# Performance work log

Measured on AMD Instinct MI355X. Metric: run time of the kernel, lower is better.

Reference implementation:

```python
import jax, jax.numpy as jnp
import numpy as np

B, K, H, W = 4096, 8, 64, 64   # z: [B, K, H, W], K = n_bits
S = 50                          # min(50, H*W*K) random sites sampled
HID = 64
CTX = 9 * K - 1                 # 3x3 neighborhood * K bits, minus the center-self bit


def setup_inputs() -> dict:
    key = jax.random.key(0)
    kz, k1, k2, kb, ki, kj = jax.random.split(key, 6)
    # z is a field of bits (0/1) as floats, as the (pred != z) comparison implies
    z = (jax.random.uniform(kz, (B, K, H, W)) > 0.5).astype(jnp.float32)
    W1 = jax.random.normal(k1, (CTX, HID), dtype=jnp.float32) * (1.0 / np.sqrt(CTX))
    b1 = jnp.zeros((HID,), dtype=jnp.float32)
    W2 = jax.random.normal(k2, (HID,), dtype=jnp.float32) * (1.0 / np.sqrt(HID))
    b2 = jnp.zeros((), dtype=jnp.float32)
    # the 50 random (bit, row, col) triples, precomputed (replaces torch.randint().item() loop)
    b_idx = jax.random.randint(kb, (S,), 0, K)
    i_idx = jax.random.randint(ki, (S,), 0, H)
    j_idx = jax.random.randint(kj, (S,), 0, W)
    return {"z": z, "W1": W1, "b1": b1, "W2": W2, "b2": b2,
            "b_idx": b_idx, "i_idx": i_idx, "j_idx": j_idx}


def reference(z, W1, b1, W2, b2, b_idx, i_idx, j_idx):
    # 3x3 toroidal neighborhood offsets, in the same (di outer, dj inner) order as the torch loop
    di = jnp.repeat(jnp.array([-1, 0, 1]), 3)          # [9]
    dj = jnp.tile(jnp.array([-1, 0, 1]), 3)            # [9]
    ni = (i_idx[:, None] + di[None, :]) % H            # [S, 9]
    nj = (j_idx[:, None] + dj[None, :]) % W            # [S, 9]

    # gather neighborhoods for all samples at once: [B, K, S, 9]
    neigh = z[:, :, ni, nj]
    # torch ctx ordering: position-major (di,dj), bit-minor -> [B, S, 9, K] -> [B, S, 9K]
    ctx_full = jnp.transpose(neigh, (0, 2, 3, 1)).reshape(z.shape[0], S, 9 * K)

    # drop the center-self entry at flat index 4*K + b (center position is the 5th of 9)
    drop = 4 * K + b_idx                               # [S]
    t = jnp.arange(CTX)                                # [CTX]
    gidx = t[None, :] + (t[None, :] >= drop[:, None])  # [S, CTX], skips `drop` per sample
    ctx = jnp.take_along_axis(ctx_full, gidx[None, :, :], axis=2)  # [B, S, CTX]

    # tiny 2-layer MLP predictor, batched over all B*S contexts
    h = jax.nn.relu(jnp.einsum('bsc,ch->bsh', ctx, W1) + b1)       # [B, S, HID]
    logits = jnp.einsum('bsh,h->bs', h, W2) + b2                   # [B, S]
    pred = (logits > 0).astype(z.dtype)

    target = z[:, b_idx, i_idx, j_idx]                             # [B, S]
    v = (pred != target).astype(z.dtype).mean(axis=0)              # [S] per-sample violation rate
    return v.mean()
```

## Files before the change

kernel.cpp:

```cpp
#include <hip/hip_runtime.h>

#define NB   4096
#define NK   8
#define NH   64
#define NW   64
#define NS   50
#define NHID 64
#define NCTX 71


__device__ __forceinline__ int getbit(const unsigned long long* bits, int cell) {
    int word = ((cell >> 8) << 2) | (cell & 3);
    int bit  = (cell >> 2) & 63;
    return (int)((bits[word] >> bit) & 1ull);
}

__global__ __launch_bounds__(256, 4)
void local_energy_kernel(const float* __restrict__ z,
                         const float* __restrict__ W1,
                         const float* __restrict__ b1,
                         const float* __restrict__ W2,
                         const float* __restrict__ b2,
                         const int*   __restrict__ b_idx,
                         const int*   __restrict__ i_idx,
                         const int*   __restrict__ j_idx,
                         float*       __restrict__ out)
{
    __shared__ unsigned long long bits[512];
    __shared__ float blocksum[4];

    const int tid  = threadIdx.x;
    const int lane = tid & 63;
    const int wave = tid >> 6;
    const int b    = blockIdx.x;

    const float4* src = (const float4*)(z + (size_t)b * (NK * NH * NW));
    for (int outer = 0; outer < 8; ++outer) {
        float4 v[4];
        #pragma unroll
        for (int q = 0; q < 4; ++q)
            v[q] = src[(outer * 4 + q) * 256 + tid];
        #pragma unroll
        for (int q = 0; q < 4; ++q) {
            int iter = outer * 4 + q;
            unsigned long long m0 = __ballot(v[q].x > 0.5f);
            unsigned long long m1 = __ballot(v[q].y > 0.5f);
            unsigned long long m2 = __ballot(v[q].z > 0.5f);
            unsigned long long m3 = __ballot(v[q].w > 0.5f);
            if (lane == 0) {
                int g = (iter << 2) | wave;
                bits[(g << 2) | 0] = m0;
                bits[(g << 2) | 1] = m1;
                bits[(g << 2) | 2] = m2;
                bits[(g << 2) | 3] = m3;
            }
        }
    }
    __syncthreads();

    float W1c[NCTX];
    #pragma unroll
    for (int t = 0; t < NCTX; ++t) W1c[t] = W1[t * NHID + lane];
    const float b1v = b1[lane];
    const float W2v = W2[lane];
    const float b2v = b2[0];

    float miss = 0.0f;
    for (int s = wave; s < NS; s += 4) {
        const int bb = b_idx[s];
        const int ii = i_idx[s];
        const int jj = j_idx[s];

        int u  = lane;
        int p  = u >> 3, k = u & 7;
        int di = p / 3, dj = p - di * 3;
        int ni = (ii + di - 1) & (NH - 1);
        int nj = (jj + dj - 1) & (NW - 1);
        int cell = (k << 12) | (ni << 6) | nj;
        unsigned long long lo = __ballot(getbit(bits, cell) != 0);

        int k2  = lane & 7;
        int ni2 = (ii + 1) & (NH - 1);
        int nj2 = (jj + 1) & (NW - 1);
        int cell2 = (k2 << 12) | (ni2 << 6) | nj2;
        int bv2 = (lane < 8) ? getbit(bits, cell2) : 0;
        unsigned long long hi = __ballot(bv2 != 0) & 0xffull;

        const int drop = 32 + bb;
        unsigned long long mlo = (lo & ((1ull << drop) - 1ull))
                               | ((lo >> (drop + 1)) << drop)
                               | ((hi & 1ull) << 63);
        unsigned int mhi = (unsigned int)(hi >> 1);

        float h0 = b1v, h1 = 0.0f, h2 = 0.0f, h3 = 0.0f;
        #pragma unroll
        for (int t = 0; t < 64; t += 4) {
            h0 += ((mlo >> (t + 0)) & 1ull) ? W1c[t + 0] : 0.0f;
            h1 += ((mlo >> (t + 1)) & 1ull) ? W1c[t + 1] : 0.0f;
            h2 += ((mlo >> (t + 2)) & 1ull) ? W1c[t + 2] : 0.0f;
            h3 += ((mlo >> (t + 3)) & 1ull) ? W1c[t + 3] : 0.0f;
        }
        #pragma unroll
        for (int t = 0; t < 7; ++t)
            h0 += ((mhi >> t) & 1u) ? W1c[64 + t] : 0.0f;
        float h = fmaxf((h0 + h1) + (h2 + h3), 0.0f);

        float c = h * W2v;
        #pragma unroll
        for (int off = 32; off >= 1; off >>= 1)
            c += __shfl_xor(c, off, 64);
        float logit = c + b2v;

        int pred = (logit > 0.0f) ? 1 : 0;
        int cellT = (bb << 12) | (ii << 6) | jj;
        int targ  = getbit(bits, cellT);
        if (lane == 0) miss += (float)(pred != targ);
    }

    if (lane == 0) blocksum[wave] = miss;
    __syncthreads();
    if (tid == 0) {
        float tot = (blocksum[0] + blocksum[1]) + (blocksum[2] + blocksum[3]);
        atomicAdd(out, tot * (1.0f / (float)(NB * NS)));
    }
}

extern "C" void kernel_launch(void* const* d_in, const int* in_sizes, int n_in,
                              void* d_out, int out_size, void* d_ws, size_t ws_size,
                              hipStream_t stream) {
    const float* z    = (const float*)d_in[0];
    const float* W1   = (const float*)d_in[1];
    const float* b1   = (const float*)d_in[2];
    const float* W2   = (const float*)d_in[3];
    const float* b2   = (const float*)d_in[4];
    const int*   b_i  = (const int*)d_in[5];
    const int*   i_i  = (const int*)d_in[6];
    const int*   j_i  = (const int*)d_in[7];
    float* out = (float*)d_out;

    hipMemsetAsync(out, 0, sizeof(float), stream);

    local_energy_kernel<<<NB, 256, 0, stream>>>(z, W1, b1, W2, b2, b_i, i_i, j_i, out);
}
```

Before: 737.0 us.

## Use nontemporal z loads, stage sample indices in LDS, two-pass reduction

Loads of z now use nontemporal loads because each element is read only once, which spares cache pollution. The sample indices are staged once per block into shared memory and the per-lane neighborhood offsets are hoisted out of the loop. The memset plus 4096 global atomics are replaced by per-block partials written to the workspace and a second single-block reduction kernel. This adds an extra kernel launch. The kernel is bound by streaming 512 MB of z, so the gains are likely marginal.

```diff
diff --git a/kernel.cpp b/kernel.cpp
--- a/kernel.cpp
+++ b/kernel.cpp
@@ -8,6 +8,7 @@
 #define NHID 64
 #define NCTX 71
 
+typedef float f32x4 __attribute__((ext_vector_type(4)));
 
 __device__ __forceinline__ int getbit(const unsigned long long* bits, int cell) {
     int word = ((cell >> 8) << 2) | (cell & 3);
@@ -24,9 +25,10 @@
                          const int*   __restrict__ b_idx,
                          const int*   __restrict__ i_idx,
                          const int*   __restrict__ j_idx,
-                         float*       __restrict__ out)
+                         float*       __restrict__ partials)
 {
     __shared__ unsigned long long bits[512];
+    __shared__ int   sidx[3][NS];
     __shared__ float blocksum[4];
 
     const int tid  = threadIdx.x;
@@ -34,19 +36,25 @@
     const int wave = tid >> 6;
     const int b    = blockIdx.x;
 
-    const float4* src = (const float4*)(z + (size_t)b * (NK * NH * NW));
+    if (tid < 3 * NS) {
+        int a = tid / NS, r = tid - a * NS;
+        const int* p = (a == 0) ? b_idx : (a == 1) ? i_idx : j_idx;
+        sidx[a][r] = p[r];
+    }
+
+    const f32x4* src = (const f32x4*)(z + (size_t)b * (NK * NH * NW));
     for (int outer = 0; outer < 8; ++outer) {
-        float4 v[4];
+        f32x4 v[4];
         #pragma unroll
         for (int q = 0; q < 4; ++q)
-            v[q] = src[(outer * 4 + q) * 256 + tid];
+            v[q] = __builtin_nontemporal_load(&src[(outer * 4 + q) * 256 + tid]);
         #pragma unroll
         for (int q = 0; q < 4; ++q) {
             int iter = outer * 4 + q;
-            unsigned long long m0 = __ballot(v[q].x > 0.5f);
-            unsigned long long m1 = __ballot(v[q].y > 0.5f);
-            unsigned long long m2 = __ballot(v[q].z > 0.5f);
-            unsigned long long m3 = __ballot(v[q].w > 0.5f);
+            unsigned long long m0 = __ballot(v[q][0] > 0.5f);
+            unsigned long long m1 = __ballot(v[q][1] > 0.5f);
+            unsigned long long m2 = __ballot(v[q][2] > 0.5f);
+            unsigned long long m3 = __ballot(v[q][3] > 0.5f);
             if (lane == 0) {
                 int g = (iter << 2) | wave;
                 bits[(g << 2) | 0] = m0;
@@ -65,24 +73,24 @@
     const float W2v = W2[lane];
     const float b2v = b2[0];
 
+    const int p  = lane >> 3;
+    const int kk = lane & 7;
+    const int di = p / 3, dj = p - di * 3;
+
     float miss = 0.0f;
     for (int s = wave; s < NS; s += 4) {
-        const int bb = b_idx[s];
-        const int ii = i_idx[s];
-        const int jj = j_idx[s];
+        const int bb = sidx[0][s];
+        const int ii = sidx[1][s];
+        const int jj = sidx[2][s];
 
-        int u  = lane;
-        int p  = u >> 3, k = u & 7;
-        int di = p / 3, dj = p - di * 3;
         int ni = (ii + di - 1) & (NH - 1);
         int nj = (jj + dj - 1) & (NW - 1);
-        int cell = (k << 12) | (ni << 6) | nj;
+        int cell = (kk << 12) | (ni << 6) | nj;
         unsigned long long lo = __ballot(getbit(bits, cell) != 0);
 
-        int k2  = lane & 7;
         int ni2 = (ii + 1) & (NH - 1);
         int nj2 = (jj + 1) & (NW - 1);
-        int cell2 = (k2 << 12) | (ni2 << 6) | nj2;
+        int cell2 = ((lane & 7) << 12) | (ni2 << 6) | nj2;
         int bv2 = (lane < 8) ? getbit(bits, cell2) : 0;
         unsigned long long hi = __ballot(bv2 != 0) & 0xffull;
 
@@ -119,10 +127,30 @@
 
     if (lane == 0) blocksum[wave] = miss;
     __syncthreads();
-    if (tid == 0) {
-        float tot = (blocksum[0] + blocksum[1]) + (blocksum[2] + blocksum[3]);
-        atomicAdd(out, tot * (1.0f / (float)(NB * NS)));
-    }
+    if (tid == 0)
+        partials[b] = (blocksum[0] + blocksum[1]) + (blocksum[2] + blocksum[3]);
+}
+
+__global__ __launch_bounds__(256)
+void reduce_kernel(const float* __restrict__ partials, float* __restrict__ out)
+{
+    __shared__ float wsum[4];
+    const int tid  = threadIdx.x;
+    const int lane = tid & 63;
+    const int wave = tid >> 6;
+
+    float s = 0.0f;
+    #pragma unroll
+    for (int q = 0; q < NB / 256; ++q)
+        s += partials[q * 256 + tid];
+    #pragma unroll
+    for (int off = 32; off >= 1; off >>= 1)
+        s += __shfl_xor(s, off, 64);
+    if (lane == 0) wsum[wave] = s;
+    __syncthreads();
+    if (tid == 0)
+        out[0] = ((wsum[0] + wsum[1]) + (wsum[2] + wsum[3]))
+                 * (1.0f / (float)(NB * NS));
 }
 
 extern "C" void kernel_launch(void* const* d_in, const int* in_sizes, int n_in,
@@ -136,9 +164,9 @@
     const int*   b_i  = (const int*)d_in[5];
     const int*   i_i  = (const int*)d_in[6];
     const int*   j_i  = (const int*)d_in[7];
-    float* out = (float*)d_out;
+    float* out      = (float*)d_out;
+    float* partials = (float*)d_ws;
 
-    hipMemsetAsync(out, 0, sizeof(float), stream);
-
-    local_energy_kernel<<<NB, 256, 0, stream>>>(z, W1, b1, W2, b2, b_i, i_i, j_i, out);
+    local_energy_kernel<<<NB, 256, 0, stream>>>(z, W1, b1, W2, b2, b_i, i_i, j_i, partials);
+    reduce_kernel<<<1, 256, 0, stream>>>(partials, out);
 }
```

Result: faster. 714.0 us (-3.1%).
